# Optimization experiments

Hardware: AMD Instinct MI355X
Metric: run time of the kernel (lower is better)

The kernel has to match this reference:

```python
import jax, jax.numpy as jnp
import numpy as np

N, M, D = 256, 64, 1024


def _l2norm(x, axis=-1, eps=1e-12):
    # tf.math.l2_normalize semantics: x / sqrt(max(sum(x^2), eps))
    sq = jnp.sum(x * x, axis=axis, keepdims=True)
    return x * jax.lax.rsqrt(jnp.maximum(sq, eps))


def setup_inputs() -> dict:
    key = jax.random.key(0)
    k1, = jax.random.split(key, 1)
    inputs = jax.random.normal(k1, (N * M, D), dtype=jnp.float32)
    w = jnp.full((1,), 10.0, dtype=jnp.float32)
    b = jnp.full((1,), -5.0, dtype=jnp.float32)
    return {"inputs": inputs, "w": w, "b": b}


def reference(inputs, w, b):
    emb = inputs.reshape(N, M, D)                       # (N, M, D)
    # speaker centroids (normalized mean over utterances)
    center = _l2norm(jnp.mean(emb, axis=1))             # (N, D)
    # leave-one-out centroid per utterance: sum over M minus self (NOT divided)
    center_except = _l2norm(jnp.sum(emb, axis=1, keepdims=True) - emb)  # (N, M, D)
    # off-diagonal similarities: every utterance vs every speaker centroid
    sim_all = jnp.einsum('jmd,id->jmi', emb, center)    # (N_utt_spk j, M, N_centroid i)
    # diagonal (i == j): utterance vs its own leave-one-out centroid
    diag = jnp.sum(center_except * emb, axis=-1)        # (N, M)
    eye = jnp.eye(N, dtype=bool)[:, None, :]            # (N, 1, N)
    sim = jnp.where(eye, diag[:, :, None], sim_all)     # (N, M, N)
    sim = w * sim + b
    return sim.reshape(N * M, N)
```

## Files before the change

### kernel.cpp

```cpp
#include <hip/hip_runtime.h>

#define NSPK 256
#define MUTT 64
#define DDIM 1024
#define NROW (NSPK * MUTT)

using frag_ab = __attribute__((ext_vector_type(8))) short;
using frag_cd = __attribute__((ext_vector_type(4))) float;

static __device__ __forceinline__ unsigned short f32_to_bf16(float f) {
    unsigned int u = __float_as_uint(f);
    return (unsigned short)((u + 0x7FFFu + ((u >> 16) & 1u)) >> 16);
}
static __device__ __forceinline__ unsigned int pack2(float a, float b) {
    return (unsigned)f32_to_bf16(a) | ((unsigned)f32_to_bf16(b) << 16);
}
static __device__ __forceinline__ void gload16(const void* g, void* l) {
    __builtin_amdgcn_global_load_lds(
        (const __attribute__((address_space(1))) unsigned int*)g,
        (__attribute__((address_space(3))) unsigned int*)l, 16, 0, 0);
}


__global__ void __launch_bounds__(256) k_prep(const float* __restrict__ emb,
                                              float* __restrict__ Sp,
                                              unsigned short* __restrict__ ebf,
                                              float* __restrict__ qg) {
    const int j = blockIdx.x;
    const int h = blockIdx.y;
    const int t = threadIdx.x;
    const int lane = t & 63, wave = t >> 6;
    const size_t rowbase = (size_t)j * MUTT + (size_t)h * 8;
    const float* src = emb + rowbase * DDIM + (size_t)t * 4;
    unsigned short* edst = ebf + rowbase * DDIM + (size_t)t * 4;
    __shared__ float qws[8][4];
    float4 s = make_float4(0.f, 0.f, 0.f, 0.f);
    #pragma unroll
    for (int m = 0; m < 8; ++m) {
        float4 v = *(const float4*)(src + (size_t)m * DDIM);
        s.x += v.x; s.y += v.y; s.z += v.z; s.w += v.w;
        float qp = v.x * v.x + v.y * v.y + v.z * v.z + v.w * v.w;
        #pragma unroll
        for (int off = 32; off > 0; off >>= 1) qp += __shfl_down(qp, off, 64);
        if (lane == 0) qws[m][wave] = qp;
        *(uint2*)(edst + (size_t)m * DDIM) = make_uint2(pack2(v.x, v.y), pack2(v.z, v.w));
    }
    __syncthreads();
    if (t < 8) qg[rowbase + t] = qws[t][0] + qws[t][1] + qws[t][2] + qws[t][3];
    *(float4*)(Sp + ((size_t)h * NSPK + j) * DDIM + (size_t)t * 4) = s;
}

template <int P>
__global__ void k_center(const float* __restrict__ Sp, unsigned short* __restrict__ cbf,
                         float* __restrict__ normS2g, float* __restrict__ normSg) {
    const int j = blockIdx.x;
    const int t = threadIdx.x;
    float4 v = make_float4(0.f, 0.f, 0.f, 0.f);
    #pragma unroll
    for (int p = 0; p < P; ++p) {
        float4 a = *(const float4*)(Sp + ((size_t)p * NSPK + j) * DDIM + (size_t)t * 4);
        v.x += a.x; v.y += a.y; v.z += a.z; v.w += a.w;
    }
    float sq = v.x * v.x + v.y * v.y + v.z * v.z + v.w * v.w;
    #pragma unroll
    for (int off = 32; off > 0; off >>= 1) sq += __shfl_down(sq, off, 64);
    __shared__ float ws[4];
    __shared__ float sc_sh;
    const int lane = t & 63, wave = t >> 6;
    if (lane == 0) ws[wave] = sq;
    __syncthreads();
    if (t == 0) {
        float tot = ws[0] + ws[1] + ws[2] + ws[3];
        normS2g[j] = tot;
        normSg[j]  = sqrtf(tot);
        float msq = tot * (1.0f / 4096.0f);
        sc_sh = rsqrtf(fmaxf(msq, 1e-12f)) * (1.0f / 64.0f);
    }
    __syncthreads();
    const float sc = sc_sh;
    *(uint2*)(cbf + (size_t)j * DDIM + (size_t)t * 4) =
        make_uint2(pack2(v.x * sc, v.y * sc), pack2(v.z * sc, v.w * sc));
}

__global__ void __launch_bounds__(256, 2)
k_gemm5(const unsigned short* __restrict__ ebf, const unsigned short* __restrict__ cbf,
        const float* __restrict__ qg, const float* __restrict__ n2g,
        const float* __restrict__ n1g,
        const float* __restrict__ wp, const float* __restrict__ bp,
        float* __restrict__ out) {
    __shared__ unsigned short Bs[64 * 512];

    const int tid = threadIdx.x, lane = tid & 63, wave = tid >> 6;
    const int bx = blockIdx.x;
    const int ct = blockIdx.y;
    const int row0 = bx * 128;
    const int c0 = ct * 64;

    const int quad = lane >> 4;
    const int m16 = lane & 15;

    const char* agbase = (const char*)ebf + ((size_t)(row0 + wave * 32 + m16) * DDIM + quad * 8) * 2;

    frag_cd acc[2][4];
    #pragma unroll
    for (int rr = 0; rr < 2; ++rr)
        #pragma unroll
        for (int cc = 0; cc < 4; ++cc) acc[rr][cc] = (frag_cd){0.f, 0.f, 0.f, 0.f};

    #pragma unroll
    for (int h = 0; h < 2; ++h) {
        if (h) __syncthreads();
        #pragma unroll
        for (int round = 0; round < 16; ++round) {
            const int col = round * 4 + wave;
            const int s = col & 7;
            const char* g = (const char*)cbf +
                (size_t)(c0 + col) * (DDIM * 2) + h * 1024 + ((lane ^ s) << 4);
            gload16(g, (char*)Bs + col * 1024 + (lane << 4));
        }
        __syncthreads();

        #pragma unroll 4
        for (int ks = 0; ks < 16; ++ks) {
            frag_ab af[2], bf[4];
            const int koff = h * 1024 + ks * 64;
            af[0] = *(const frag_ab*)(agbase + koff);
            af[1] = *(const frag_ab*)(agbase + 16 * (DDIM * 2) + koff);
            #pragma unroll
            for (int cc = 0; cc < 4; ++cc) {
                const int col = cc * 16 + m16;
                const int chunk = ((ks * 4 + quad) ^ (col & 7));
                bf[cc] = *(const frag_ab*)((const char*)Bs + col * 1024 + (chunk << 4));
            }
            #pragma unroll
            for (int rr = 0; rr < 2; ++rr)
                #pragma unroll
                for (int cc = 0; cc < 4; ++cc)
                    acc[rr][cc] = __builtin_amdgcn_mfma_f32_16x16x32_bf16(
                        af[rr], bf[cc], acc[rr][cc], 0, 0, 0);
        }
    }

    const float wv = wp[0], bv = bp[0];
    #pragma unroll
    for (int rr = 0; rr < 2; ++rr) {
        int rbase = wave * 32 + rr * 16 + (quad << 2);
        #pragma unroll
        for (int cc = 0; cc < 4; ++cc) {
            int col = c0 + cc * 16 + m16;
            frag_cd v = acc[rr][cc];
            #pragma unroll
            for (int r2 = 0; r2 < 4; ++r2) {
                int grow = row0 + rbase + r2;
                float val = v[r2];
                int jspk = grow >> 6;
                if (col == jspk) {
                    float q = qg[grow];
                    float ns2 = n2g[jspk];
                    float ns = n1g[jspk];
                    float rd = val * ns;
                    float den2 = ns2 - 2.f * rd + q;
                    val = (rd - q) * rsqrtf(fmaxf(den2, 1e-12f));
                }
                out[(size_t)grow * NSPK + col] = wv * val + bv;
            }
        }
    }
}


__global__ void k_sums(const float* __restrict__ emb, float* __restrict__ Sp) {
    const int j = blockIdx.x;
    const int h = blockIdx.y;
    const int c = threadIdx.x;
    const float* base = emb + ((size_t)j * MUTT + (size_t)h * 32) * DDIM + (size_t)c * 4;
    float4 acc = make_float4(0.f, 0.f, 0.f, 0.f);
    #pragma unroll 8
    for (int m = 0; m < 32; ++m) {
        float4 v = *(const float4*)(base + (size_t)m * DDIM);
        acc.x += v.x; acc.y += v.y; acc.z += v.z; acc.w += v.w;
    }
    *(float4*)(Sp + ((size_t)h * NSPK + j) * DDIM + (size_t)c * 4) = acc;
}

__global__ void __launch_bounds__(256)
k_gemm_old(const float* __restrict__ emb, const unsigned short* __restrict__ cbf,
           const float* __restrict__ normS2g, const float* __restrict__ normSg,
           const float* __restrict__ wp, const float* __restrict__ bp,
           float* __restrict__ out) {
    __shared__ unsigned short Asm[32][32];
    __shared__ unsigned short Bsm[256][32];
    __shared__ float qpart[32][8];
    __shared__ float qfin[32];
    const int tid = threadIdx.x, lane = tid & 63, wave = tid >> 6;
    const int row0 = blockIdx.x * 32;
    const int jspk = row0 >> 6;
    frag_cd acc[2][4];
    #pragma unroll
    for (int rr = 0; rr < 2; ++rr)
        #pragma unroll
        for (int cc = 0; cc < 4; ++cc) acc[rr][cc] = (frag_cd){0.f, 0.f, 0.f, 0.f};
    const int ar = tid >> 3, ak = (tid & 7) << 2;
    const float* aptr = emb + (size_t)(row0 + ar) * DDIM + ak;
    float qacc = 0.f;
    const int bi = tid >> 2, bk = (tid & 3) << 3;
    const int am = lane & 15, kq = (lane >> 4) << 3;
    for (int k0 = 0; k0 < DDIM; k0 += 32) {
        __syncthreads();
        float4 av = *(const float4*)(aptr + k0);
        qacc += av.x * av.x + av.y * av.y + av.z * av.z + av.w * av.w;
        *(uint2*)&Asm[ar][ak] = make_uint2(pack2(av.x, av.y), pack2(av.z, av.w));
        #pragma unroll
        for (int p = 0; p < 4; ++p) {
            int brow = p * 64 + bi;
            *(uint4*)&Bsm[brow][bk] = *(const uint4*)(cbf + (size_t)brow * DDIM + k0 + bk);
        }
        __syncthreads();
        frag_ab afr[2], bfr[4];
        #pragma unroll
        for (int rr = 0; rr < 2; ++rr) afr[rr] = *(const frag_ab*)&Asm[rr * 16 + am][kq];
        #pragma unroll
        for (int cc = 0; cc < 4; ++cc) bfr[cc] = *(const frag_ab*)&Bsm[wave * 64 + cc * 16 + am][kq];
        #pragma unroll
        for (int rr = 0; rr < 2; ++rr)
            #pragma unroll
            for (int cc = 0; cc < 4; ++cc)
                acc[rr][cc] = __builtin_amdgcn_mfma_f32_16x16x32_bf16(afr[rr], bfr[cc], acc[rr][cc], 0, 0, 0);
    }
    qpart[ar][tid & 7] = qacc;
    __syncthreads();
    if (tid < 32) {
        float s = 0.f;
        #pragma unroll
        for (int u = 0; u < 8; ++u) s += qpart[tid][u];
        qfin[tid] = s;
    }
    __syncthreads();
    const float wv = wp[0], bv = bp[0];
    const float ns2 = normS2g[jspk], ns = normSg[jspk];
    #pragma unroll
    for (int rr = 0; rr < 2; ++rr) {
        int rbase = rr * 16 + ((lane >> 4) << 2);
        #pragma unroll
        for (int cc = 0; cc < 4; ++cc) {
            int col = wave * 64 + cc * 16 + (lane & 15);
            frag_cd v = acc[rr][cc];
            #pragma unroll
            for (int r2 = 0; r2 < 4; ++r2) {
                int lrow = rbase + r2;
                float val = v[r2];
                if (col == jspk) {
                    float q = qfin[lrow];
                    float rd = val * ns;
                    float den2 = ns2 - 2.f * rd + q;
                    val = (rd - q) * rsqrtf(fmaxf(den2, 1e-12f));
                }
                out[(size_t)(row0 + lrow) * NSPK + col] = wv * val + bv;
            }
        }
    }
}

extern "C" void kernel_launch(void* const* d_in, const int* in_sizes, int n_in,
                              void* d_out, int out_size, void* d_ws, size_t ws_size,
                              hipStream_t stream) {
    const float* emb = (const float*)d_in[0];
    const float* w   = (const float*)d_in[1];
    const float* b   = (const float*)d_in[2];
    float* out = (float*)d_out;

    const size_t sz_Sp  = (size_t)8 * NSPK * DDIM * 4;
    const size_t sz_ebf = (size_t)NROW * DDIM * 2;
    const size_t sz_cbf = (size_t)NSPK * DDIM * 2;
    const size_t sz_qg  = (size_t)NROW * 4;
    const size_t need = sz_Sp + sz_ebf + sz_cbf + sz_qg + 2 * NSPK * 4;

    if (ws_size >= need) {
        char* p = (char*)d_ws;
        float* Sp = (float*)p;              p += sz_Sp;
        unsigned short* ebf = (unsigned short*)p; p += sz_ebf;
        unsigned short* cbf = (unsigned short*)p; p += sz_cbf;
        float* qg = (float*)p;              p += sz_qg;
        float* n2 = (float*)p;              p += NSPK * 4;
        float* n1 = n2 + NSPK;
        k_prep<<<dim3(NSPK, 8), 256, 0, stream>>>(emb, Sp, ebf, qg);
        k_center<8><<<NSPK, 256, 0, stream>>>(Sp, cbf, n2, n1);
        k_gemm5<<<dim3(NROW / 128, NSPK / 64), 256, 0, stream>>>(ebf, cbf, qg, n2, n1, w, b, out);
    } else {
        float* Sp = (float*)d_ws;
        unsigned short* cbf = (unsigned short*)(Sp + 2 * NSPK * DDIM);
        float* n2 = (float*)(cbf + NSPK * DDIM);
        float* n1 = n2 + NSPK;
        k_sums<<<dim3(NSPK, 2), 256, 0, stream>>>(emb, Sp);
        k_center<2><<<NSPK, 256, 0, stream>>>(Sp, cbf, n2, n1);
        k_gemm_old<<<NROW / 32, 256, 0, stream>>>(emb, cbf, n2, n1, w, b, out);
    }
}
```

Baseline: 130.6 us.

## Restructure GEMM to stage A rows in LDS and stream centroids from registers

The GEMM kernel now gives each block a 32-row A tile held in LDS, staged with swizzled direct-to-LDS loads, and covers all 256 centroid columns, one 64-column slab per wave. B fragments come straight from global/L2 through a 3-deep register prefetch ring, replacing the earlier B-in-LDS tile with per-half syncs. Because each block sits inside one speaker, the diagonal epilogue loads the norms once instead of per element. Separately, the prep kernel handles 16 rows per block instead of 8, which halves the partial-sum buffer and the center kernel's reduction. This trades LDS reuse of B for heavier L2 traffic on B and a larger LDS footprint per block.

```diff
diff --git a/kernel.cpp b/kernel.cpp
--- a/kernel.cpp
+++ b/kernel.cpp
@@ -30,13 +30,13 @@
     const int h = blockIdx.y;
     const int t = threadIdx.x;
     const int lane = t & 63, wave = t >> 6;
-    const size_t rowbase = (size_t)j * MUTT + (size_t)h * 8;
+    const size_t rowbase = (size_t)j * MUTT + (size_t)h * 16;
     const float* src = emb + rowbase * DDIM + (size_t)t * 4;
     unsigned short* edst = ebf + rowbase * DDIM + (size_t)t * 4;
-    __shared__ float qws[8][4];
+    __shared__ float qws[16][4];
     float4 s = make_float4(0.f, 0.f, 0.f, 0.f);
     #pragma unroll
-    for (int m = 0; m < 8; ++m) {
+    for (int m = 0; m < 16; ++m) {
         float4 v = *(const float4*)(src + (size_t)m * DDIM);
         s.x += v.x; s.y += v.y; s.z += v.z; s.w += v.w;
         float qp = v.x * v.x + v.y * v.y + v.z * v.z + v.w * v.w;
@@ -46,7 +46,7 @@
         *(uint2*)(edst + (size_t)m * DDIM) = make_uint2(pack2(v.x, v.y), pack2(v.z, v.w));
     }
     __syncthreads();
-    if (t < 8) qg[rowbase + t] = qws[t][0] + qws[t][1] + qws[t][2] + qws[t][3];
+    if (t < 16) qg[rowbase + t] = qws[t][0] + qws[t][1] + qws[t][2] + qws[t][3];
     *(float4*)(Sp + ((size_t)h * NSPK + j) * DDIM + (size_t)t * 4) = s;
 }
 
@@ -83,23 +83,34 @@
 }
 
 __global__ void __launch_bounds__(256, 2)
-k_gemm5(const unsigned short* __restrict__ ebf, const unsigned short* __restrict__ cbf,
+k_gemm6(const unsigned short* __restrict__ ebf, const unsigned short* __restrict__ cbf,
         const float* __restrict__ qg, const float* __restrict__ n2g,
         const float* __restrict__ n1g,
         const float* __restrict__ wp, const float* __restrict__ bp,
         float* __restrict__ out) {
-    __shared__ unsigned short Bs[64 * 512];
+    __shared__ unsigned short As[32 * DDIM];
 
     const int tid = threadIdx.x, lane = tid & 63, wave = tid >> 6;
-    const int bx = blockIdx.x;
-    const int ct = blockIdx.y;
-    const int row0 = bx * 128;
-    const int c0 = ct * 64;
-
+    const int row0 = blockIdx.x * 32;
     const int quad = lane >> 4;
     const int m16 = lane & 15;
 
-    const char* agbase = (const char*)ebf + ((size_t)(row0 + wave * 32 + m16) * DDIM + quad * 8) * 2;
+    {
+        const char* ag = (const char*)(ebf + (size_t)row0 * DDIM);
+        #pragma unroll
+        for (int r = 0; r < 16; ++r) {
+            const int c = r * 256 + tid;
+            const int rw = c >> 7;
+            const int p = c & 127;
+            gload16(ag + rw * 2048 + ((p ^ (rw & 7)) << 4),
+                    (char*)As + rw * 2048 + (p << 4));
+        }
+    }
+
+    const char* bg[4];
+    #pragma unroll
+    for (int cc = 0; cc < 4; ++cc)
+        bg[cc] = (const char*)cbf + (size_t)(wave * 64 + cc * 16 + m16) * 2048 + quad * 16;
 
     frag_cd acc[2][4];
     #pragma unroll
@@ -107,57 +118,52 @@
         #pragma unroll
         for (int cc = 0; cc < 4; ++cc) acc[rr][cc] = (frag_cd){0.f, 0.f, 0.f, 0.f};
 
-    #pragma unroll
-    for (int h = 0; h < 2; ++h) {
-        if (h) __syncthreads();
-        #pragma unroll
-        for (int round = 0; round < 16; ++round) {
-            const int col = round * 4 + wave;
-            const int s = col & 7;
-            const char* g = (const char*)cbf +
-                (size_t)(c0 + col) * (DDIM * 2) + h * 1024 + ((lane ^ s) << 4);
-            gload16(g, (char*)Bs + col * 1024 + (lane << 4));
-        }
-        __syncthreads();
-
-        #pragma unroll 4
-        for (int ks = 0; ks < 16; ++ks) {
-            frag_ab af[2], bf[4];
-            const int koff = h * 1024 + ks * 64;
-            af[0] = *(const frag_ab*)(agbase + koff);
-            af[1] = *(const frag_ab*)(agbase + 16 * (DDIM * 2) + koff);
-            #pragma unroll
-            for (int cc = 0; cc < 4; ++cc) {
-                const int col = cc * 16 + m16;
-                const int chunk = ((ks * 4 + quad) ^ (col & 7));
-                bf[cc] = *(const frag_ab*)((const char*)Bs + col * 1024 + (chunk << 4));
-            }
-            #pragma unroll
-            for (int rr = 0; rr < 2; ++rr)
-                #pragma unroll
-                for (int cc = 0; cc < 4; ++cc)
-                    acc[rr][cc] = __builtin_amdgcn_mfma_f32_16x16x32_bf16(
-                        af[rr], bf[cc], acc[rr][cc], 0, 0, 0);
-        }
+    frag_ab bf[3][4];
+    #pragma unroll
+    for (int cc = 0; cc < 4; ++cc) bf[0][cc] = *(const frag_ab*)(bg[cc]);
+    #pragma unroll
+    for (int cc = 0; cc < 4; ++cc) bf[1][cc] = *(const frag_ab*)(bg[cc] + 64);
+
+    __syncthreads();
+
+    #pragma unroll
+    for (int ks = 0; ks < 32; ++ks) {
+        if (ks + 2 < 32) {
+            #pragma unroll
+            for (int cc = 0; cc < 4; ++cc)
+                bf[(ks + 2) % 3][cc] = *(const frag_ab*)(bg[cc] + (ks + 2) * 64);
+        }
+        frag_ab af[2];
+        #pragma unroll
+        for (int rr = 0; rr < 2; ++rr) {
+            const int rw = rr * 16 + m16;
+            const int chunk = (ks * 4 + quad) ^ (rw & 7);
+            af[rr] = *(const frag_ab*)((const char*)As + rw * 2048 + (chunk << 4));
+        }
+        #pragma unroll
+        for (int rr = 0; rr < 2; ++rr)
+            #pragma unroll
+            for (int cc = 0; cc < 4; ++cc)
+                acc[rr][cc] = __builtin_amdgcn_mfma_f32_16x16x32_bf16(
+                    af[rr], bf[ks % 3][cc], acc[rr][cc], 0, 0, 0);
     }
 
     const float wv = wp[0], bv = bp[0];
+    const int jspk = row0 >> 6;
+    const float ns2 = n2g[jspk], ns = n1g[jspk];
     #pragma unroll
     for (int rr = 0; rr < 2; ++rr) {
-        int rbase = wave * 32 + rr * 16 + (quad << 2);
+        int rbase = rr * 16 + (quad << 2);
         #pragma unroll
         for (int cc = 0; cc < 4; ++cc) {
-            int col = c0 + cc * 16 + m16;
+            int col = wave * 64 + cc * 16 + m16;
             frag_cd v = acc[rr][cc];
             #pragma unroll
             for (int r2 = 0; r2 < 4; ++r2) {
                 int grow = row0 + rbase + r2;
                 float val = v[r2];
-                int jspk = grow >> 6;
                 if (col == jspk) {
                     float q = qg[grow];
-                    float ns2 = n2g[jspk];
-                    float ns = n1g[jspk];
                     float rd = val * ns;
                     float den2 = ns2 - 2.f * rd + q;
                     val = (rd - q) * rsqrtf(fmaxf(den2, 1e-12f));
@@ -269,7 +275,7 @@
     const float* b   = (const float*)d_in[2];
     float* out = (float*)d_out;
 
-    const size_t sz_Sp  = (size_t)8 * NSPK * DDIM * 4;
+    const size_t sz_Sp  = (size_t)4 * NSPK * DDIM * 4;
     const size_t sz_ebf = (size_t)NROW * DDIM * 2;
     const size_t sz_cbf = (size_t)NSPK * DDIM * 2;
     const size_t sz_qg  = (size_t)NROW * 4;
@@ -283,9 +289,9 @@
         float* qg = (float*)p;              p += sz_qg;
         float* n2 = (float*)p;              p += NSPK * 4;
         float* n1 = n2 + NSPK;
-        k_prep<<<dim3(NSPK, 8), 256, 0, stream>>>(emb, Sp, ebf, qg);
-        k_center<8><<<NSPK, 256, 0, stream>>>(Sp, cbf, n2, n1);
-        k_gemm5<<<dim3(NROW / 128, NSPK / 64), 256, 0, stream>>>(ebf, cbf, qg, n2, n1, w, b, out);
+        k_prep<<<dim3(NSPK, 4), 256, 0, stream>>>(emb, Sp, ebf, qg);
+        k_center<4><<<NSPK, 256, 0, stream>>>(Sp, cbf, n2, n1);
+        k_gemm6<<<NROW / 32, 256, 0, stream>>>(ebf, cbf, qg, n2, n1, w, b, out);
     } else {
         float* Sp = (float*)d_ws;
         unsigned short* cbf = (unsigned short*)(Sp + 2 * NSPK * DDIM);
```

Result: slower. 148.5 us (+13.7%).
